# Kernel optimization log

Hardware: AMD Instinct MI355X
Metric: run time of the kernel (lower is better)

Reference implementation:

```python
import jax, jax.numpy as jnp
import numpy as np

D, H, HD, F, A, P, NB, MD = 1024, 16, 64, 2816, 64, 30, 32, 128
B, L = 4, 1024


def _rel_bucket(rel, num_buckets=NB, max_distance=MD):
    # T5 relative position bucket, bidirectional=False (decoder self-attn)
    rel = -jnp.minimum(rel, 0)
    max_exact = num_buckets // 2
    is_small = rel < max_exact
    large = max_exact + (
        jnp.log(jnp.maximum(rel, 1).astype(jnp.float32) / max_exact)
        / np.log(max_distance / max_exact)
        * (num_buckets - max_exact)
    ).astype(jnp.int32)
    large = jnp.minimum(large, num_buckets - 1)
    return jnp.where(is_small, rel, large)


def _rmsnorm(x, scale, eps=1e-6):
    var = jnp.mean(jnp.square(x), axis=-1, keepdims=True)
    return x * jax.lax.rsqrt(var + eps) * scale


def _attn(x, kv, wq, wk, wv, wo, mask, bias, pk, pv):
    # x: [B,Lq,D], kv: [B,Lk,D], prefix pk/pv: [B,P,H,HD]
    hd = wq.shape[-1]
    q = jnp.einsum('bqd,dhe->bqhe', x, wq) * (hd ** -0.5)
    k = jnp.einsum('bkd,dhe->bkhe', kv, wk)
    v = jnp.einsum('bkd,dhe->bkhe', kv, wv)
    k = jnp.concatenate([pk, k], axis=1)  # prefix KV prepended
    v = jnp.concatenate([pv, v], axis=1)
    logits = jnp.einsum('bqhe,bkhe->bhqk', q, k).astype(jnp.float32)
    p = pk.shape[1]
    if bias is not None:
        logits = logits + jnp.pad(bias, ((0, 0), (0, 0), (0, 0), (p, 0)))
    mask = jnp.pad(mask, ((0, 0), (0, 0), (0, 0), (p, 0)), constant_values=True)
    logits = jnp.where(mask, logits, jnp.float32(-1e10))
    w = jax.nn.softmax(logits, axis=-1).astype(x.dtype)
    o = jnp.einsum('bhqk,bkhe->bqhe', w, v)
    return jnp.einsum('bqhe,hed->bqd', o, wo)


def setup_inputs() -> dict:
    key = jax.random.key(0)
    ks = jax.random.split(key, 24)
    s = D ** -0.5
    inp = {
        'inputs': jax.random.normal(ks[0], (B, L, D), jnp.float32),
        'encoded': jax.random.normal(ks[1], (B, L, D), jnp.float32),
        'adapter_wd': jax.random.normal(ks[2], (B, D, A), jnp.float32) * s,
        'adapter_wu': jax.random.normal(ks[3], (B, A, D), jnp.float32) * (A ** -0.5),
        'adapter_bd': jax.random.normal(ks[4], (B, A), jnp.float32) * 0.02,
        'adapter_bu': jax.random.normal(ks[5], (B, D), jnp.float32) * 0.02,
        'prefix_key': jax.random.normal(ks[6], (B, 2, P, H, HD), jnp.float32),
        'prefix_value': jax.random.normal(ks[7], (B, 2, P, H, HD), jnp.float32),
        'ln1': jnp.ones((D,), jnp.float32),
        'ln2': jnp.ones((D,), jnp.float32),
        'ln3': jnp.ones((D,), jnp.float32),
        'sa_wq': jax.random.normal(ks[8], (D, H, HD), jnp.float32) * s,
        'sa_wk': jax.random.normal(ks[9], (D, H, HD), jnp.float32) * s,
        'sa_wv': jax.random.normal(ks[10], (D, H, HD), jnp.float32) * s,
        'sa_wo': jax.random.normal(ks[11], (H, HD, D), jnp.float32) * s,
        'ca_wq': jax.random.normal(ks[12], (D, H, HD), jnp.float32) * s,
        'ca_wk': jax.random.normal(ks[13], (D, H, HD), jnp.float32) * s,
        'ca_wv': jax.random.normal(ks[14], (D, H, HD), jnp.float32) * s,
        'ca_wo': jax.random.normal(ks[15], (H, HD, D), jnp.float32) * s,
        'relpos': jax.random.normal(ks[16], (H, NB), jnp.float32) * 0.1,
        'mlp_wi0': jax.random.normal(ks[17], (D, F), jnp.float32) * s,
        'mlp_wi1': jax.random.normal(ks[18], (D, F), jnp.float32) * s,
        'mlp_wo': jax.random.normal(ks[19], (F, D), jnp.float32) * (F ** -0.5),
        'decoder_mask': jnp.broadcast_to(jnp.tril(jnp.ones((L, L), bool))[None, None], (B, 1, L, L)),
        'encoder_decoder_mask': jnp.ones((B, 1, L, L), bool),
    }
    return inp


def reference(inputs, encoded, adapter_wd, adapter_wu, adapter_bd, adapter_bu,
              prefix_key, prefix_value, ln1, ln2, ln3,
              sa_wq, sa_wk, sa_wv, sa_wo, ca_wq, ca_wk, ca_wv, ca_wo,
              relpos, mlp_wi0, mlp_wi1, mlp_wo,
              decoder_mask, encoder_decoder_mask):
    l = inputs.shape[1]
    pos = jnp.arange(l)
    buckets = _rel_bucket(pos[None, :] - pos[:, None])  # [L,L]
    bias = relpos[:, buckets][None]                      # [1,H,L,L]
    # self-attention with prefix + relative bias
    x = _rmsnorm(inputs, ln1)
    x = _attn(x, x, sa_wq, sa_wk, sa_wv, sa_wo, decoder_mask, bias,
              prefix_key[:, 0], prefix_value[:, 0])
    x = x + inputs
    # cross-attention with prefix
    y = _rmsnorm(x, ln2)
    y = _attn(y, encoded, ca_wq, ca_wk, ca_wv, ca_wo, encoder_decoder_mask, None,
              prefix_key[:, 1], prefix_value[:, 1])
    y = y + x
    # gated-gelu MLP + per-example adapter
    lz = _rmsnorm(y, ln3)
    z = (jax.nn.gelu(lz @ mlp_wi0) * (lz @ mlp_wi1)) @ mlp_wo
    az = jnp.einsum('bld,bda->bla', lz, adapter_wd) + adapter_bd[:, None]
    az = jax.nn.gelu(az)
    az = jnp.einsum('bla,bad->bld', az, adapter_wu) + adapter_bu[:, None]
    z = z + az
    return z + y
```

## Files before the change

kernel.cpp:

```cpp
#include <hip/hip_runtime.h>

typedef unsigned short u16;
typedef __attribute__((ext_vector_type(8))) __bf16 bf16x8;
typedef __attribute__((ext_vector_type(4))) float f32x4;

__device__ __forceinline__ float bf2f(u16 u) {
  union { unsigned int i; float f; } v; v.i = ((unsigned int)u) << 16; return v.f;
}
__device__ __forceinline__ u16 f2bf(float f) {
  unsigned int x = __float_as_uint(f);
  unsigned int r = (x + 0x7fffu + ((x >> 16) & 1u)) >> 16;
  return (u16)r;
}
__device__ __forceinline__ float gelu_f(float x) {
  float u = 0.7978845608028654f * (x + 0.044715f * x * x * x);
  float t = 1.0f - 2.0f / (__expf(2.0f * u) + 1.0f);
  return 0.5f * x * (1.0f + t);
}
__device__ __forceinline__ void gl_lds16(const u16* g, u16* l) {
  __builtin_amdgcn_global_load_lds(
      (const __attribute__((address_space(1))) unsigned int*)g,
      (__attribute__((address_space(3))) unsigned int*)l, 16, 0, 0);
}

__global__ __launch_bounds__(256) void cast_bf16_k(const float* __restrict__ in,
                                                   u16* __restrict__ out, int n4) {
  int i = blockIdx.x * 256 + threadIdx.x;
  if (i >= n4) return;
  float4 v = ((const float4*)in)[i];
  ushort4 o;
  o.x = f2bf(v.x); o.y = f2bf(v.y); o.z = f2bf(v.z); o.w = f2bf(v.w);
  ((ushort4*)out)[i] = o;
}

__global__ __launch_bounds__(256) void transpose_k(
    const float* __restrict__ in, u16* __restrict__ out, int R, int C,
    long isb, long osb) {
  __shared__ u16 tile[32][33];
  in += (size_t)blockIdx.z * isb;
  out += (size_t)blockIdx.z * osb;
  int c0 = blockIdx.x * 32, r0 = blockIdx.y * 32;
  int tx = threadIdx.x & 31, ty = threadIdx.x >> 5;
#pragma unroll
  for (int i = 0; i < 4; ++i) {
    int rr = r0 + ty + i * 8;
    if (rr < R && c0 + tx < C) tile[ty + i * 8][tx] = f2bf(in[(size_t)rr * C + c0 + tx]);
  }
  __syncthreads();
#pragma unroll
  for (int i = 0; i < 4; ++i) {
    int cc = c0 + ty + i * 8;
    if (cc < C && r0 + tx < R) out[(size_t)cc * R + r0 + tx] = tile[tx][ty + i * 8];
  }
}

__global__ __launch_bounds__(256) void bias_tab_k(const float* __restrict__ relpos,
                                                  float* __restrict__ tab) {
  int idx = blockIdx.x * 256 + threadIdx.x;
  int h = idx >> 10, d = idx & 1023;
  int bucket;
  if (d < 16) bucket = d;
  else {
    int lb = 16 + (int)(logf((float)d * (1.0f / 16.0f)) * (16.0f / logf(8.0f)));
    bucket = lb < 31 ? lb : 31;
  }
  tab[idx] = relpos[h * 32 + bucket];
}

__global__ __launch_bounds__(256) void prefix_fill_k(
    const float* __restrict__ pK, const float* __restrict__ pV,
    u16* __restrict__ Kd, u16* __restrict__ Vtd, int sSel) {
  int idx = blockIdx.x * 256 + threadIdx.x;
  int e = idx & 63, p = (idx >> 6) & 31, h = (idx >> 11) & 15, b = idx >> 15;
  int key = (p < 30) ? p : (1024 + p);
  float kv = 0.f, vv = 0.f;
  if (p < 30) {
    size_t src = ((((size_t)(b * 2 + sSel)) * 30 + p) * 16 + h) * 64 + e;
    kv = pK[src]; vv = pV[src];
  }
  Kd[(((size_t)(b * 16 + h)) * 1056 + key) * 64 + e] = f2bf(kv);
  Vtd[(((size_t)(b * 16 + h)) * 64 + e) * 1056 + key] = f2bf(vv);
}

__global__ __launch_bounds__(256) void rmsnorm_k(const float* __restrict__ in,
                                                 const float* __restrict__ scale,
                                                 u16* __restrict__ out) {
  const int D = 1024;
  size_t base = (size_t)blockIdx.x * D;
  int t = threadIdx.x;
  float x[4];
#pragma unroll
  for (int i = 0; i < 4; ++i) x[i] = in[base + t + i * 256];
  float s = x[0] * x[0] + x[1] * x[1] + x[2] * x[2] + x[3] * x[3];
#pragma unroll
  for (int off = 1; off < 64; off <<= 1) s += __shfl_xor(s, off, 64);
  __shared__ float ws4[4];
  if ((t & 63) == 0) ws4[t >> 6] = s;
  __syncthreads();
  float tot = ws4[0] + ws4[1] + ws4[2] + ws4[3];
  float r = rsqrtf(tot * (1.0f / D) + 1e-6f);
#pragma unroll
  for (int i = 0; i < 4; ++i) {
    int c = t + i * 256;
    out[base + c] = f2bf(x[i] * r * scale[c]);
  }
}

__global__ __launch_bounds__(256) void gelumul_k(const u16* __restrict__ g2,
                                                 u16* __restrict__ g) {
  int i = blockIdx.x * 256 + threadIdx.x;
  int m = i / 352, f8 = i - m * 352;
  size_t b0 = (size_t)m * 5632 + f8 * 8;
  uint4 h0 = *(const uint4*)(g2 + b0);
  uint4 h1 = *(const uint4*)(g2 + b0 + 2816);
  const u16* p0 = (const u16*)&h0;
  const u16* p1 = (const u16*)&h1;
  uint4 ov;
  u16* po = (u16*)&ov;
#pragma unroll
  for (int j = 0; j < 8; ++j) po[j] = f2bf(gelu_f(bf2f(p0[j])) * bf2f(p1[j]));
  *(uint4*)(g + (size_t)m * 2816 + f8 * 8) = ov;
}

template <int MODE>
__global__ __launch_bounds__(256) void gemm97(
    const u16* __restrict__ A, const u16* __restrict__ Bt, void* __restrict__ out,
    void* __restrict__ out2, void* __restrict__ out3,
    const float* __restrict__ res1, int M, int N, int K, float alpha) {
  const int BK = 32;
  __shared__ __align__(16) u16 As[128 * 32];
  __shared__ __align__(16) u16 Bs[128 * 32];

  const int t = threadIdx.x;
  const int wave = t >> 6, lane = t & 63;
  const int m0 = blockIdx.y * 128, n0 = blockIdx.x * 128;
  const int fr = lane & 15, fq = lane >> 4;
  const int wm = (wave >> 1) * 64, wn = (wave & 1) * 64;

  const int srow = wave * 32 + (lane >> 2);
  const int scol = (lane & 3) * 8;
  const u16* ag0 = A + (size_t)(m0 + srow) * K + scol;
  const u16* ag1 = ag0 + (size_t)16 * K;
  const u16* bg0 = Bt + (size_t)(n0 + srow) * K + scol;
  const u16* bg1 = bg0 + (size_t)16 * K;
  u16* al0 = &As[(wave * 32) * 32];
  u16* al1 = &As[(wave * 32 + 16) * 32];
  u16* bl0 = &Bs[(wave * 32) * 32];
  u16* bl1 = &Bs[(wave * 32 + 16) * 32];

  f32x4 acc[16];
#pragma unroll
  for (int i = 0; i < 16; ++i) acc[i] = (f32x4){0.f, 0.f, 0.f, 0.f};

  for (int k0 = 0; k0 < K; k0 += BK) {
    gl_lds16(ag0 + k0, al0);
    gl_lds16(ag1 + k0, al1);
    gl_lds16(bg0 + k0, bl0);
    gl_lds16(bg1 + k0, bl1);
    __syncthreads();
    bf16x8 af[4], bf[4];
#pragma unroll
    for (int i = 0; i < 4; ++i)
      af[i] = *(const bf16x8*)&As[(wm + i * 16 + fr) * 32 + fq * 8];
#pragma unroll
    for (int j = 0; j < 4; ++j)
      bf[j] = *(const bf16x8*)&Bs[(wn + j * 16 + fr) * 32 + fq * 8];
#pragma unroll
    for (int i = 0; i < 4; ++i)
#pragma unroll
      for (int j = 0; j < 4; ++j)
        acc[i * 4 + j] = __builtin_amdgcn_mfma_f32_16x16x32_bf16(
            af[i], bf[j], acc[i * 4 + j], 0, 0, 0);
    __syncthreads();
  }

#pragma unroll
  for (int i = 0; i < 4; ++i) {
#pragma unroll
    for (int rr = 0; rr < 4; ++rr) {
      long gm = (long)m0 + wm + i * 16 + fq * 4 + rr;
#pragma unroll
      for (int j = 0; j < 4; ++j) {
        int gn = n0 + wn + j * 16 + fr;
        float v = acc[i * 4 + j][rr];
        size_t oi = (size_t)gm * N + gn;
        if (MODE == 0) ((float*)out)[oi] = v;
        if (MODE == 2) ((u16*)out)[oi] = f2bf(v);
        if (MODE == 3) ((float*)out)[oi] = v + res1[oi];
        if (MODE == 8) {
          int b = (int)(gm >> 10), l = (int)(gm & 1023), h = gn >> 6, e = gn & 63;
          ((u16*)out)[(((size_t)(b * 16 + h)) * 1024 + l) * 64 + e] = f2bf(v * alpha);
        }
        if (MODE == 11) {
          int b = (int)(gm >> 10), l = (int)(gm & 1023);
          int sec = gn >> 10, nn = gn & 1023, h = nn >> 6, e = nn & 63;
          if (sec == 0)
            ((u16*)out)[(((size_t)(b * 16 + h)) * 1024 + l) * 64 + e] = f2bf(v * alpha);
          else if (sec == 1)
            ((u16*)out2)[(((size_t)(b * 16 + h)) * 1056 + 30 + l) * 64 + e] = f2bf(v);
          else
            ((u16*)out3)[(((size_t)(b * 16 + h)) * 64 + e) * 1056 + 30 + l] = f2bf(v);
        }
        if (MODE == 12) {
          int b = (int)(gm >> 10), l = (int)(gm & 1023);
          int sec = gn >> 10, nn = gn & 1023, h = nn >> 6, e = nn & 63;
          if (sec == 0)
            ((u16*)out)[(((size_t)(b * 16 + h)) * 1056 + 30 + l) * 64 + e] = f2bf(v);
          else
            ((u16*)out2)[(((size_t)(b * 16 + h)) * 64 + e) * 1056 + 30 + l] = f2bf(v);
        }
      }
    }
  }
}

template <int MODE>
__global__ __launch_bounds__(256) void gemm_bt(
    const u16* __restrict__ A, const u16* __restrict__ Bt, void* __restrict__ out,
    const float* __restrict__ res1, const float* __restrict__ res2,
    const float* __restrict__ bias, int M, int N, int K,
    long Asb, long Bsb, long bsb, long r1sb, long r2sb, long osb) {
  const int BM = 128, BK = 32, LP = 40;
  __shared__ __align__(16) u16 As[BM * LP];
  __shared__ __align__(16) u16 Bs[BM * LP];

  const int t = threadIdx.x;
  const int m0 = blockIdx.y * BM;
  const int n0 = blockIdx.x * 128;
  const int bz = blockIdx.z;
  A += (size_t)bz * Asb;
  Bt += (size_t)bz * Bsb;

  f32x4 acc[16];
#pragma unroll
  for (int i = 0; i < 16; ++i) acc[i] = (f32x4){0.f, 0.f, 0.f, 0.f};
  const int wave = t >> 6, lane = t & 63;
  const int wm = (wave >> 1) * 64, wn = (wave & 1) * 64;
  const int fr = lane & 15, fq = lane >> 4;

  for (int k0 = 0; k0 < K; k0 += BK) {
#pragma unroll
    for (int i = 0; i < 2; ++i) {
      int idx = (i * 256 + t) * 8;
      int row = idx >> 5, col = idx & 31;
      *(uint4*)&As[row * LP + col] =
          *(const uint4*)(A + (size_t)(m0 + row) * K + k0 + col);
      uint4 bv = {0u, 0u, 0u, 0u};
      if (n0 + row < N) bv = *(const uint4*)(Bt + (size_t)(n0 + row) * K + k0 + col);
      *(uint4*)&Bs[row * LP + col] = bv;
    }
    __syncthreads();
    bf16x8 af[4], bfr[4];
#pragma unroll
    for (int i = 0; i < 4; ++i)
      af[i] = *(const bf16x8*)&As[(wm + i * 16 + fr) * LP + fq * 8];
#pragma unroll
    for (int j = 0; j < 4; ++j)
      bfr[j] = *(const bf16x8*)&Bs[(wn + j * 16 + fr) * LP + fq * 8];
#pragma unroll
    for (int i = 0; i < 4; ++i)
#pragma unroll
      for (int j = 0; j < 4; ++j)
        acc[i * 4 + j] = __builtin_amdgcn_mfma_f32_16x16x32_bf16(
            af[i], bfr[j], acc[i * 4 + j], 0, 0, 0);
    __syncthreads();
  }

#pragma unroll
  for (int i = 0; i < 4; ++i) {
#pragma unroll
    for (int rr = 0; rr < 4; ++rr) {
      long gm = (long)m0 + wm + i * 16 + fq * 4 + rr;
#pragma unroll
      for (int j = 0; j < 4; ++j) {
        int gn = n0 + wn + j * 16 + fr;
        if (gn >= N) continue;
        float v = acc[i * 4 + j][rr];
        size_t oi = (size_t)bz * osb + (size_t)gm * N + gn;
        size_t ri = (size_t)gm * N + gn;
        if (MODE == 6) ((u16*)out)[oi] = f2bf(gelu_f(v + bias[(size_t)bz * bsb + gn]));
        if (MODE == 7)
          ((float*)out)[oi] = v + bias[(size_t)bz * bsb + gn] +
                              res1[(size_t)bz * r1sb + ri] +
                              res2[(size_t)bz * r2sb + ri];
      }
    }
  }
}

template <bool IS_SELF>
__global__ __launch_bounds__(256) void fattn_k(
    const u16* __restrict__ Qg, const u16* __restrict__ Kg,
    const u16* __restrict__ Vtg, const float* __restrict__ bias_tab,
    u16* __restrict__ Out) {
  const int L = 1024, P = 30, KC = 1056;
  const int b = blockIdx.z, h = blockIdx.y, q0b = blockIdx.x * 64;
  const int t = threadIdx.x, wave = t >> 6, lane = t & 63;
  const int fr = lane & 15, fq = lane >> 4;
  const int q0w = q0b + wave * 16;

  __shared__ __align__(16) u16 Ks[32][72];
  __shared__ __align__(16) u16 Vts[64][40];
  __shared__ __align__(16) u16 Ps[4][16][40];

  const u16* qptr = Qg + (((size_t)(b * 16 + h)) * L + q0w + fr) * 64 + fq * 8;
  bf16x8 qa0 = *(const bf16x8*)qptr;
  bf16x8 qa1 = *(const bf16x8*)(qptr + 32);

  f32x4 o[4];
#pragma unroll
  for (int i = 0; i < 4; ++i) o[i] = (f32x4){0.f, 0.f, 0.f, 0.f};
  float m[4] = {-3.0e38f, -3.0e38f, -3.0e38f, -3.0e38f};
  float l[4] = {0.f, 0.f, 0.f, 0.f};

  const int nk = IS_SELF ? (P + q0b + 64) : (P + L);
  const int nch = (nk + 31) >> 5;
  const size_t kbase = ((size_t)(b * 16 + h)) * KC * 64;
  const size_t vbase = ((size_t)(b * 16 + h)) * 64 * KC;

  const int skk = t >> 3, sdd = (t & 7) * 8;
  const int svd = t >> 2, svo = (t & 3) * 8;

  for (int ch = 0; ch < nch; ++ch) {
    const int k0 = ch * 32;
    *(uint4*)&Ks[skk][sdd] = *(const uint4*)(Kg + kbase + (size_t)(k0 + skk) * 64 + sdd);
    *(uint4*)&Vts[svd][svo] = *(const uint4*)(Vtg + vbase + (size_t)svd * KC + k0 + svo);
    __syncthreads();

    f32x4 s[2];
    s[0] = (f32x4){0.f, 0.f, 0.f, 0.f};
    s[1] = (f32x4){0.f, 0.f, 0.f, 0.f};
#pragma unroll
    for (int t2 = 0; t2 < 2; ++t2) {
      bf16x8 kb0 = *(const bf16x8*)&Ks[t2 * 16 + fr][fq * 8];
      bf16x8 kb1 = *(const bf16x8*)&Ks[t2 * 16 + fr][32 + fq * 8];
      s[t2] = __builtin_amdgcn_mfma_f32_16x16x32_bf16(qa0, kb0, s[t2], 0, 0, 0);
      s[t2] = __builtin_amdgcn_mfma_f32_16x16x32_bf16(qa1, kb1, s[t2], 0, 0, 0);
    }

#pragma unroll
    for (int reg = 0; reg < 4; ++reg) {
      const int qq = q0w + fq * 4 + reg;
#pragma unroll
      for (int t2 = 0; t2 < 2; ++t2) {
        const int kvi = k0 + t2 * 16 + fr;
        float sv = s[t2][reg];
        if (IS_SELF) {
          const int lk = kvi - P;
          if (lk >= 0) {
            if (lk <= qq) sv += bias_tab[h * 1024 + (qq - lk)];
            else sv = -3.0e38f;
          }
        } else {
          if (kvi >= P + L) sv = -3.0e38f;
        }
        s[t2][reg] = sv;
      }
      float a = fmaxf(s[0][reg], s[1][reg]);
      a = fmaxf(a, __shfl_xor(a, 1, 16));
      a = fmaxf(a, __shfl_xor(a, 2, 16));
      a = fmaxf(a, __shfl_xor(a, 4, 16));
      a = fmaxf(a, __shfl_xor(a, 8, 16));
      float mn = fmaxf(m[reg], a);
      float al = __expf(m[reg] - mn);
      m[reg] = mn;
      float p0 = __expf(s[0][reg] - mn);
      float p1 = __expf(s[1][reg] - mn);
      s[0][reg] = p0; s[1][reg] = p1;
      float ps = p0 + p1;
      ps += __shfl_xor(ps, 1, 16);
      ps += __shfl_xor(ps, 2, 16);
      ps += __shfl_xor(ps, 4, 16);
      ps += __shfl_xor(ps, 8, 16);
      l[reg] = l[reg] * al + ps;
#pragma unroll
      for (int dt = 0; dt < 4; ++dt) o[dt][reg] *= al;
    }

#pragma unroll
    for (int reg = 0; reg < 4; ++reg) {
#pragma unroll
      for (int t2 = 0; t2 < 2; ++t2)
        Ps[wave][fq * 4 + reg][t2 * 16 + fr] = f2bf(s[t2][reg]);
    }
    bf16x8 pa = *(const bf16x8*)&Ps[wave][fr][fq * 8];

#pragma unroll
    for (int dt = 0; dt < 4; ++dt) {
      bf16x8 vbf = *(const bf16x8*)&Vts[dt * 16 + fr][fq * 8];
      o[dt] = __builtin_amdgcn_mfma_f32_16x16x32_bf16(pa, vbf, o[dt], 0, 0, 0);
    }
    __syncthreads();
  }

  float inv[4];
#pragma unroll
  for (int reg = 0; reg < 4; ++reg) inv[reg] = 1.0f / l[reg];
#pragma unroll
  for (int dt = 0; dt < 4; ++dt) {
#pragma unroll
    for (int reg = 0; reg < 4; ++reg) {
      size_t oidx =
          (((size_t)(b * L + q0w + fq * 4 + reg)) * 16 + h) * 64 + dt * 16 + fr;
      Out[oidx] = f2bf(o[dt][reg] * inv[reg]);
    }
  }
}

extern "C" void kernel_launch(void* const* d_in, const int* in_sizes, int n_in,
                              void* d_out, int out_size, void* d_ws, size_t ws_size,
                              hipStream_t stream) {
  const int B = 4, L = 1024, D = 1024, H = 16, F = 2816, AD = 64;
  const int M = B * L;
  const int KC = 1056;

  const float* inputs  = (const float*)d_in[0];
  const float* encoded = (const float*)d_in[1];
  const float* a_wd    = (const float*)d_in[2];
  const float* a_wu    = (const float*)d_in[3];
  const float* a_bd    = (const float*)d_in[4];
  const float* a_bu    = (const float*)d_in[5];
  const float* pK      = (const float*)d_in[6];
  const float* pV      = (const float*)d_in[7];
  const float* ln1     = (const float*)d_in[8];
  const float* ln2     = (const float*)d_in[9];
  const float* ln3     = (const float*)d_in[10];
  const float* sa_wq   = (const float*)d_in[11];
  const float* sa_wk   = (const float*)d_in[12];
  const float* sa_wv   = (const float*)d_in[13];
  const float* sa_wo   = (const float*)d_in[14];
  const float* ca_wq   = (const float*)d_in[15];
  const float* ca_wk   = (const float*)d_in[16];
  const float* ca_wv   = (const float*)d_in[17];
  const float* ca_wo   = (const float*)d_in[18];
  const float* relpos  = (const float*)d_in[19];
  const float* wi0     = (const float*)d_in[20];
  const float* wi1     = (const float*)d_in[21];
  const float* wom     = (const float*)d_in[22];

  char* w = (char*)d_ws;
  size_t used = 0;
  auto alloc = [&](size_t bytes) {
    char* p = w + used;
    used += (bytes + 255) & ~(size_t)255;
    return p;
  };
  u16* wqkvT  = (u16*)alloc((size_t)3072 * 1024 * 2);
  u16* woT    = (u16*)alloc((size_t)D * 1024 * 2);
  u16* cqT    = (u16*)alloc((size_t)D * 1024 * 2);
  u16* ckvT   = (u16*)alloc((size_t)2048 * 1024 * 2);
  u16* coT    = (u16*)alloc((size_t)D * 1024 * 2);
  u16* wi01T  = (u16*)alloc((size_t)5632 * 1024 * 2);
  u16* womT   = (u16*)alloc((size_t)D * F * 2);
  u16* wdT    = (u16*)alloc((size_t)B * AD * D * 2);
  u16* wuT    = (u16*)alloc((size_t)B * D * AD * 2);
  float* bT   = (float*)alloc((size_t)H * 1024 * 4);
  u16* enc16  = (u16*)alloc((size_t)M * D * 2);
  u16* xn     = (u16*)alloc((size_t)M * D * 2);
  u16* lz     = (u16*)alloc((size_t)M * D * 2);
  u16* Kc     = (u16*)alloc((size_t)B * H * KC * 64 * 2);
  u16* Vtc    = (u16*)alloc((size_t)B * H * 64 * KC * 2);
  u16* qh     = (u16*)alloc((size_t)B * H * L * 64 * 2);
  u16* ao     = (u16*)alloc((size_t)M * D * 2);
  float* xf   = (float*)alloc((size_t)M * D * 4);
  float* yf   = (float*)alloc((size_t)M * D * 4);
  u16* az1    = (u16*)alloc((size_t)B * 1024 * AD * 2);
  u16* g2     = Kc;
  u16* g      = enc16;
  float* zf   = (float*)Kc;
  if (used > ws_size) return;

  dim3 tb(256);
  auto T = [&](const float* src, u16* dst, int R, int C, int nb, long sb) {
    transpose_k<<<dim3((C + 31) / 32, (R + 31) / 32, nb), tb, 0, stream>>>(
        src, dst, R, C, sb, sb);
  };
  T(sa_wq, wqkvT, D, 1024, 1, 0);
  T(sa_wk, wqkvT + (size_t)1024 * 1024, D, 1024, 1, 0);
  T(sa_wv, wqkvT + (size_t)2048 * 1024, D, 1024, 1, 0);
  T(sa_wo, woT, 1024, D, 1, 0);
  T(ca_wq, cqT, D, 1024, 1, 0);
  T(ca_wk, ckvT, D, 1024, 1, 0);
  T(ca_wv, ckvT + (size_t)1024 * 1024, D, 1024, 1, 0);
  T(ca_wo, coT, 1024, D, 1, 0);
  T(wi0, wi01T, D, F, 1, 0);
  T(wi1, wi01T + (size_t)2816 * 1024, D, F, 1, 0);
  T(wom, womT, F, D, 1, 0);
  T(a_wd, wdT, D, AD, B, (long)D * AD);
  T(a_wu, wuT, AD, D, B, (long)AD * D);
  bias_tab_k<<<dim3(64), tb, 0, stream>>>(relpos, bT);
  cast_bf16_k<<<dim3(M * D / 4 / 256), tb, 0, stream>>>(encoded, enc16, M * D / 4);

#define G97(MODE, Ap, Btp, Op, O2, O3, R1, Nn, Kk, al)                         \
  gemm97<MODE><<<dim3((Nn) / 128, M / 128), tb, 0, stream>>>(                  \
      (const u16*)(Ap), (const u16*)(Btp), (void*)(Op), (void*)(O2),           \
      (void*)(O3), (const float*)(R1), M, Nn, Kk, al)

  rmsnorm_k<<<dim3(M), tb, 0, stream>>>(inputs, ln1, xn);
  G97(11, xn, wqkvT, qh, Kc, Vtc, nullptr, 3072, D, 0.125f);
  prefix_fill_k<<<dim3(512), tb, 0, stream>>>(pK, pV, Kc, Vtc, 0);
  fattn_k<true><<<dim3(L / 64, H, B), tb, 0, stream>>>(qh, Kc, Vtc, bT, ao);
  G97(3, ao, woT, xf, nullptr, nullptr, inputs, 1024, D, 1.f);
  rmsnorm_k<<<dim3(M), tb, 0, stream>>>(xf, ln2, xn);
  G97(8, xn, cqT, qh, nullptr, nullptr, nullptr, 1024, D, 0.125f);
  G97(12, enc16, ckvT, Kc, Vtc, nullptr, nullptr, 2048, D, 1.f);
  prefix_fill_k<<<dim3(512), tb, 0, stream>>>(pK, pV, Kc, Vtc, 1);
  fattn_k<false><<<dim3(L / 64, H, B), tb, 0, stream>>>(qh, Kc, Vtc, nullptr, ao);
  G97(3, ao, coT, yf, nullptr, nullptr, xf, 1024, D, 1.f);
  rmsnorm_k<<<dim3(M), tb, 0, stream>>>(yf, ln3, lz);
  gemm_bt<6><<<dim3(1, 8, B), tb, 0, stream>>>(
      lz, wdT, az1, nullptr, nullptr, a_bd, 1024, AD, D,
      (long)1024 * D, (long)AD * D, (long)AD, 0, 0, (long)1024 * AD);
  G97(2, lz, wi01T, g2, nullptr, nullptr, nullptr, 5632, D, 1.f);
  gelumul_k<<<dim3(5632), tb, 0, stream>>>(g2, g);
  G97(0, g, womT, zf, nullptr, nullptr, nullptr, 1024, F, 1.f);
  gemm_bt<7><<<dim3(8, 8, B), tb, 0, stream>>>(
      az1, wuT, d_out, zf, yf, a_bu, 1024, 1024, AD,
      (long)1024 * AD, (long)D * AD, (long)1024, (long)1024 * 1024,
      (long)1024 * 1024, (long)1024 * 1024);
#undef G97
  (void)in_sizes; (void)n_in; (void)out_size;
}
```

Before: 839.1 us.

## Load K/V fragments directly to registers with prefetch, cache bias table in LDS

```diff
diff --git a/kernel.cpp b/kernel.cpp
--- a/kernel.cpp
+++ b/kernel.cpp
@@ -299,9 +299,14 @@
   const int fr = lane & 15, fq = lane >> 4;
   const int q0w = q0b + wave * 16;
 
-  __shared__ __align__(16) u16 Ks[32][72];
-  __shared__ __align__(16) u16 Vts[64][40];
+  __shared__ float bTs[IS_SELF ? 1024 : 4];
   __shared__ __align__(16) u16 Ps[4][16][40];
+
+  if (IS_SELF) {
+#pragma unroll
+    for (int i = 0; i < 4; ++i) bTs[t + i * 256] = bias_tab[h * 1024 + t + i * 256];
+    __syncthreads();
+  }
 
   const u16* qptr = Qg + (((size_t)(b * 16 + h)) * L + q0w + fr) * 64 + fq * 8;
   bf16x8 qa0 = *(const bf16x8*)qptr;
@@ -315,47 +320,69 @@
 
   const int nk = IS_SELF ? (P + q0b + 64) : (P + L);
   const int nch = (nk + 31) >> 5;
-  const size_t kbase = ((size_t)(b * 16 + h)) * KC * 64;
-  const size_t vbase = ((size_t)(b * 16 + h)) * 64 * KC;
-
-  const int skk = t >> 3, sdd = (t & 7) * 8;
-  const int svd = t >> 2, svo = (t & 3) * 8;
+  const u16* kp = Kg + ((size_t)(b * 16 + h)) * KC * 64 + (size_t)fr * 64 + fq * 8;
+  const u16* vp = Vtg + ((size_t)(b * 16 + h)) * 64 * KC + (size_t)fr * KC + fq * 8;
+
+  bf16x8 kf0 = *(const bf16x8*)(kp + 0);
+  bf16x8 kf1 = *(const bf16x8*)(kp + 32);
+  bf16x8 kf2 = *(const bf16x8*)(kp + 16 * 64);
+  bf16x8 kf3 = *(const bf16x8*)(kp + 16 * 64 + 32);
 
   for (int ch = 0; ch < nch; ++ch) {
     const int k0 = ch * 32;
-    *(uint4*)&Ks[skk][sdd] = *(const uint4*)(Kg + kbase + (size_t)(k0 + skk) * 64 + sdd);
-    *(uint4*)&Vts[svd][svo] = *(const uint4*)(Vtg + vbase + (size_t)svd * KC + k0 + svo);
-    __syncthreads();
+    bf16x8 vf0 = *(const bf16x8*)(vp + 0 * 16 * KC + k0);
+    bf16x8 vf1 = *(const bf16x8*)(vp + 1 * 16 * KC + k0);
+    bf16x8 vf2 = *(const bf16x8*)(vp + 2 * 16 * KC + k0);
+    bf16x8 vf3 = *(const bf16x8*)(vp + 3 * 16 * KC + k0);
+    const int k0n = (ch + 1 < nch) ? (k0 + 32) : 0;
+    bf16x8 kn0 = *(const bf16x8*)(kp + (size_t)k0n * 64);
+    bf16x8 kn1 = *(const bf16x8*)(kp + (size_t)k0n * 64 + 32);
+    bf16x8 kn2 = *(const bf16x8*)(kp + (size_t)(k0n + 16) * 64);
+    bf16x8 kn3 = *(const bf16x8*)(kp + (size_t)(k0n + 16) * 64 + 32);
 
     f32x4 s[2];
     s[0] = (f32x4){0.f, 0.f, 0.f, 0.f};
     s[1] = (f32x4){0.f, 0.f, 0.f, 0.f};
-#pragma unroll
-    for (int t2 = 0; t2 < 2; ++t2) {
-      bf16x8 kb0 = *(const bf16x8*)&Ks[t2 * 16 + fr][fq * 8];
-      bf16x8 kb1 = *(const bf16x8*)&Ks[t2 * 16 + fr][32 + fq * 8];
-      s[t2] = __builtin_amdgcn_mfma_f32_16x16x32_bf16(qa0, kb0, s[t2], 0, 0, 0);
-      s[t2] = __builtin_amdgcn_mfma_f32_16x16x32_bf16(qa1, kb1, s[t2], 0, 0, 0);
+    s[0] = __builtin_amdgcn_mfma_f32_16x16x32_bf16(qa0, kf0, s[0], 0, 0, 0);
+    s[0] = __builtin_amdgcn_mfma_f32_16x16x32_bf16(qa1, kf1, s[0], 0, 0, 0);
+    s[1] = __builtin_amdgcn_mfma_f32_16x16x32_bf16(qa0, kf2, s[1], 0, 0, 0);
+    s[1] = __builtin_amdgcn_mfma_f32_16x16x32_bf16(qa1, kf3, s[1], 0, 0, 0);
+
+    const bool full = IS_SELF ? (k0 >= 32 && k0 + 31 - P <= q0w)
+                              : (k0 + 31 < P + L);
+    if (full) {
+      if (IS_SELF) {
+#pragma unroll
+        for (int reg = 0; reg < 4; ++reg) {
+          const int qq = q0w + fq * 4 + reg;
+          s[0][reg] += bTs[qq - (k0 + fr - P)];
+          s[1][reg] += bTs[qq - (k0 + 16 + fr - P)];
+        }
+      }
+    } else {
+#pragma unroll
+      for (int reg = 0; reg < 4; ++reg) {
+        const int qq = q0w + fq * 4 + reg;
+#pragma unroll
+        for (int t2 = 0; t2 < 2; ++t2) {
+          const int kvi = k0 + t2 * 16 + fr;
+          float sv = s[t2][reg];
+          if (IS_SELF) {
+            const int lk = kvi - P;
+            if (lk >= 0) {
+              if (lk <= qq) sv += bTs[qq - lk];
+              else sv = -3.0e38f;
+            }
+          } else {
+            if (kvi >= P + L) sv = -3.0e38f;
+          }
+          s[t2][reg] = sv;
+        }
+      }
     }
 
 #pragma unroll
     for (int reg = 0; reg < 4; ++reg) {
-      const int qq = q0w + fq * 4 + reg;
-#pragma unroll
-      for (int t2 = 0; t2 < 2; ++t2) {
-        const int kvi = k0 + t2 * 16 + fr;
-        float sv = s[t2][reg];
-        if (IS_SELF) {
-          const int lk = kvi - P;
-          if (lk >= 0) {
-            if (lk <= qq) sv += bias_tab[h * 1024 + (qq - lk)];
-            else sv = -3.0e38f;
-          }
-        } else {
-          if (kvi >= P + L) sv = -3.0e38f;
-        }
-        s[t2][reg] = sv;
-      }
       float a = fmaxf(s[0][reg], s[1][reg]);
       a = fmaxf(a, __shfl_xor(a, 1, 16));
       a = fmaxf(a, __shfl_xor(a, 2, 16));
@@ -379,18 +406,18 @@
 
 #pragma unroll
     for (int reg = 0; reg < 4; ++reg) {
-#pragma unroll
-      for (int t2 = 0; t2 < 2; ++t2)
-        Ps[wave][fq * 4 + reg][t2 * 16 + fr] = f2bf(s[t2][reg]);
-    }
+      Ps[wave][fq * 4 + reg][fr] = f2bf(s[0][reg]);
+      Ps[wave][fq * 4 + reg][16 + fr] = f2bf(s[1][reg]);
+    }
+    __asm__ volatile("s_waitcnt lgkmcnt(0)" ::: "memory");
     bf16x8 pa = *(const bf16x8*)&Ps[wave][fr][fq * 8];
 
-#pragma unroll
-    for (int dt = 0; dt < 4; ++dt) {
-      bf16x8 vbf = *(const bf16x8*)&Vts[dt * 16 + fr][fq * 8];
-      o[dt] = __builtin_amdgcn_mfma_f32_16x16x32_bf16(pa, vbf, o[dt], 0, 0, 0);
-    }
-    __syncthreads();
+    o[0] = __builtin_amdgcn_mfma_f32_16x16x32_bf16(pa, vf0, o[0], 0, 0, 0);
+    o[1] = __builtin_amdgcn_mfma_f32_16x16x32_bf16(pa, vf1, o[1], 0, 0, 0);
+    o[2] = __builtin_amdgcn_mfma_f32_16x16x32_bf16(pa, vf2, o[2], 0, 0, 0);
+    o[3] = __builtin_amdgcn_mfma_f32_16x16x32_bf16(pa, vf3, o[3], 0, 0, 0);
+
+    kf0 = kn0; kf1 = kn1; kf2 = kn2; kf3 = kn3;
   }
 
   float inv[4];
```

Result: no change. 840.0 us (+0.1%).
